# Performance work log

Measured on AMD Instinct MI355X. Metric: run time of the kernel, lower is better.

The kernel has to match this reference:

```python
import jax, jax.numpy as jnp
import numpy as np

N = 50000
E_G = 600000
E_K = 500000
IN_FEATS = 64
H = 128
C = 2
# calculate_theta2(d=2): Bernstein polynomial coefficients (ascending powers)
THETAS_G = [[3.0, -3.0, 0.75], [0.0, 3.0, -1.5], [0.0, 0.0, 0.75]]
THETAS_K = [[1.0, 1.0, 1.0]] * 3


def _xavier(key, shape):
    fan_in, fan_out = shape[1], shape[0]
    lim = float(np.sqrt(6.0 / (fan_in + fan_out)))
    return jax.random.uniform(key, shape, jnp.float32, -lim, lim)


def setup_inputs() -> dict:
    key = jax.random.key(0)
    ks = jax.random.split(key, 32)
    inp = {
        "x": jax.random.normal(ks[0], (N, IN_FEATS), jnp.float32),
        "src_g": jax.random.randint(ks[1], (E_G,), 0, N, jnp.int32),
        "dst_g": jax.random.randint(ks[2], (E_G,), 0, N, jnp.int32),
        "src_k": jax.random.randint(ks[3], (E_K,), 0, N, jnp.int32),
        "dst_k": jax.random.randint(ks[4], (E_K,), 0, N, jnp.int32),
        # input MLP
        "W1": _xavier(ks[5], (H, IN_FEATS)), "b1": jnp.zeros((H,), jnp.float32),
        "W2": _xavier(ks[6], (H, H)), "b2": jnp.zeros((H,), jnp.float32),
        # 3 PolyConvs on main graph: learnable_diag [3,3,H], linear [3,H,H]+bias
        "diag_g": jax.random.uniform(ks[7], (3, 3, H), jnp.float32),
        "Wc_g": jnp.stack([_xavier(ks[8 + i], (H, H)) for i in range(3)]),
        "bc_g": jnp.zeros((3, H), jnp.float32),
        # 3 PolyConvs on knn graph
        "diag_k": jax.random.uniform(ks[11], (3, 3, H), jnp.float32),
        "Wc_k": jnp.stack([_xavier(ks[12 + i], (H, H)) for i in range(3)]),
        "bc_k": jnp.zeros((3, H), jnp.float32),
        # fusion linears (3H -> H)
        "W3": _xavier(ks[15], (H, 3 * H)), "b3": jnp.zeros((H,), jnp.float32),
        "Wk": _xavier(ks[16], (H, 3 * H)), "bk": jnp.zeros((H,), jnp.float32),
        # ComponentAttention: Linear(H,H)+Tanh+Linear(H,1,no bias)
        "Wa1": _xavier(ks[17], (H, H)), "ba1": jnp.zeros((H,), jnp.float32),
        "Wa2": _xavier(ks[18], (1, H)),
        # classifier
        "W4": _xavier(ks[19], (C, H)), "b4": jnp.zeros((C,), jnp.float32),
    }
    return inp


def _dinvsqrt(dst, n):
    deg = jax.ops.segment_sum(jnp.ones(dst.shape, jnp.float32), dst, num_segments=n)
    return jnp.clip(deg, 1.0, None) ** -0.5  # [N]


def _poly_conv(feat, src, dst, dinv, theta, diag, W, b, n):
    # h = linear(theta[0]*feat * diag[0]); then k-1 Laplacian hops
    h = jnp.dot((theta[0] * feat) * diag[0], W.T) + b
    for k in range(1, len(theta)):
        m = feat * dinv  # [N,H]
        agg = jax.ops.segment_sum(m[src], dst, num_segments=n)  # SpMM
        feat = feat - (agg * dinv) * diag[k]
        h = h + theta[k] * feat
    return h


def reference(x, src_g, dst_g, src_k, dst_k, W1, b1, W2, b2, diag_g, Wc_g, bc_g,
              diag_k, Wc_k, bc_k, W3, b3, Wk, bk, Wa1, ba1, Wa2, W4, b4):
    dinv_g = _dinvsqrt(dst_g, N)[:, None]
    dinv_k = _dinvsqrt(dst_k, N)[:, None]

    h = jax.nn.relu(jnp.dot(x, W1.T) + b1)
    h = jax.nn.relu(jnp.dot(h, W2.T) + b2)

    h_o = jnp.concatenate(
        [_poly_conv(h, src_g, dst_g, dinv_g, THETAS_G[i], diag_g[i], Wc_g[i], bc_g[i], N)
         for i in range(3)], axis=-1)
    h_o = jax.nn.relu(jnp.dot(h_o, W3.T) + b3)

    h_knn = jnp.concatenate(
        [_poly_conv(h, src_k, dst_k, dinv_k, THETAS_K[i], diag_k[i], Wc_k[i], bc_k[i], N)
         for i in range(3)], axis=-1)
    h_knn = jax.nn.relu(jnp.dot(h_knn, Wk.T) + bk)

    z = jnp.stack([h_o, h_knn], axis=1)  # [N,2,H]
    w = jnp.dot(jnp.tanh(jnp.dot(z, Wa1.T) + ba1), Wa2.T)  # [N,2,1]
    beta = jax.nn.softmax(w.mean(axis=0), axis=0)  # [2,1]
    emb = (beta[None] * z).sum(axis=1)  # [N,H]

    logits = jnp.dot(emb, W4.T) + b4
    return (logits, emb)
```

## Files before the change

kernel.cpp:

```cpp
#include <hip/hip_runtime.h>
#include <math.h>

#define NN 50000
#define EG 600000
#define EK 500000
#define H 128
#define INF 64
#define NB 196

#define GRID 512

struct Theta9 { float t[9]; };

__device__ __forceinline__ float f4_at(const float4& v, int i) {
  return i == 0 ? v.x : i == 1 ? v.y : i == 2 ? v.z : v.w;
}
__device__ __forceinline__ void fma4(float4& a, float s, const float4& w) {
  a.x += s * w.x; a.y += s * w.y; a.z += s * w.z; a.w += s * w.w;
}
__device__ __forceinline__ float4 relu4(float4 a) {
  a.x = fmaxf(a.x, 0.f); a.y = fmaxf(a.y, 0.f);
  a.z = fmaxf(a.z, 0.f); a.w = fmaxf(a.w, 0.f);
  return a;
}
__device__ __forceinline__ float fast_tanh(float x) {
  float a = fabsf(x);
  float t = __expf(-2.f * a);
  float r = (1.f - t) * __builtin_amdgcn_rcpf(1.f + t);
  return copysignf(r, x);
}
__device__ __forceinline__ float dot_tanh4(const float4& w2, const float4& a) {
  return w2.x * fast_tanh(a.x) + w2.y * fast_tanh(a.y) +
         w2.z * fast_tanh(a.z) + w2.w * fast_tanh(a.w);
}

__global__ __launch_bounds__(256) void k_hist(const int* __restrict__ dg,
    const int* __restrict__ dk, int* __restrict__ cg, int* __restrict__ ck) {
  __shared__ int h[512];
  int t = threadIdx.x;
  h[t] = 0; h[t + 256] = 0;
  __syncthreads();
  for (int e = blockIdx.x * 256 + t; e < EG; e += gridDim.x * 256) {
    atomicAdd(&h[dg[e] >> 8], 1);
    if (e < EK) atomicAdd(&h[256 + (dk[e] >> 8)], 1);
  }
  __syncthreads();
  if (t < NB) {
    if (h[t]) atomicAdd(&cg[t], h[t]);
    if (h[256 + t]) atomicAdd(&ck[t], h[256 + t]);
  }
}

__global__ __launch_bounds__(256) void k_bscan(const int* __restrict__ cg,
    const int* __restrict__ ck, int* __restrict__ bg, int* __restrict__ bk,
    int* __restrict__ curg, int* __restrict__ curk,
    int* __restrict__ rpg, int* __restrict__ rpk) {
  __shared__ int sg[256], sk[256];
  int t = threadIdx.x;
  int vg = (t < NB) ? cg[t] : 0;
  int vk = (t < NB) ? ck[t] : 0;
  sg[t] = vg; sk[t] = vk;
  __syncthreads();
  for (int d = 1; d < 256; d <<= 1) {
    int ug = (t >= d) ? sg[t - d] : 0;
    int uk = (t >= d) ? sk[t - d] : 0;
    __syncthreads();
    sg[t] += ug; sk[t] += uk;
    __syncthreads();
  }
  int eg = sg[t] - vg, ek = sk[t] - vk;
  if (t < NB) {
    bg[t] = eg; bk[t] = ek;
    curg[t] = eg; curk[t] = ek;
  }
  if (t == NB - 1) {
    bg[NB] = eg + vg; bk[NB] = ek + vk;
    rpg[NN] = eg + vg; rpk[NN] = ek + vk;
  }
}

template<int E>
__global__ __launch_bounds__(256) void k_part(const int* __restrict__ src,
    const int* __restrict__ dst, int* __restrict__ gcur, int2* __restrict__ ebuf) {
  __shared__ int hist[NB], lbase[NB], cur[NB];
  int t = threadIdx.x;
  int CH = (E + gridDim.x - 1) / gridDim.x;
  int b0 = blockIdx.x * CH;
  int b1 = min(E, b0 + CH);
  if (t < NB) hist[t] = 0;
  __syncthreads();
  for (int e = b0 + t; e < b1; e += 256) atomicAdd(&hist[dst[e] >> 8], 1);
  __syncthreads();
  if (t < NB && hist[t]) lbase[t] = atomicAdd(&gcur[t], hist[t]);
  __syncthreads();
  if (t < NB) cur[t] = 0;
  __syncthreads();
  for (int e = b0 + t; e < b1; e += 256) {
    int d = dst[e];
    int b = d >> 8;
    int r = atomicAdd(&cur[b], 1);
    ebuf[lbase[b] + r] = make_int2(src[e], d);
  }
}

__global__ __launch_bounds__(256) void k_bcsr(const int2* __restrict__ ebuf,
    const int* __restrict__ bbase, int* __restrict__ rp, int* __restrict__ adj,
    float* __restrict__ dinv) {
  __shared__ int hist[256], incl[256], cur[256];
  int t = threadIdx.x, b = blockIdx.x;
  int beg = bbase[b], end = bbase[b + 1];
  int node0 = b << 8;
  int nvalid = min(256, NN - node0);
  hist[t] = 0;
  __syncthreads();
  for (int i = beg + t; i < end; i += 256) atomicAdd(&hist[ebuf[i].y - node0], 1);
  __syncthreads();
  incl[t] = hist[t];
  __syncthreads();
  for (int d = 1; d < 256; d <<= 1) {
    int u = (t >= d) ? incl[t - d] : 0;
    __syncthreads();
    incl[t] += u;
    __syncthreads();
  }
  int excl = incl[t] - hist[t];
  if (t < nvalid) {
    rp[node0 + t] = beg + excl;
    int dg = hist[t]; if (dg < 1) dg = 1;
    dinv[node0 + t] = rsqrtf((float)dg);
  }
  cur[t] = 0;
  incl[t] = excl;
  __syncthreads();
  for (int i = beg + t; i < end; i += 256) {
    int2 ed = ebuf[i];
    int d = ed.y - node0;
    int r = atomicAdd(&cur[d], 1);
    adj[beg + incl[d] + r] = ed.x;
  }
}

__global__ __launch_bounds__(256) void k_transpose(const float* __restrict__ A,
    float* __restrict__ At, int R, int C) {
  int i = blockIdx.x * 256 + threadIdx.x;
  if (i < R * C) {
    int r = i / C, c = i % C;
    At[c * R + r] = A[i];
  }
}

__global__ __launch_bounds__(256) void k_genmat(const float* __restrict__ diag,
    const float* __restrict__ Wc, const float* __restrict__ W3, Theta9 th,
    float* __restrict__ A, float* __restrict__ B, float* __restrict__ C) {
  int id = blockIdx.x * 256 + threadIdx.x;
  int k = id >> 7, j = id & 127;
  float a = 0.f, b = 0.f, c = 0.f;
  for (int i = 0; i < 3; i++) {
    float t0 = th.t[i * 3 + 0], t1 = th.t[i * 3 + 1], t2 = th.t[i * 3 + 2];
    float d0 = diag[(i * 3 + 0) * H + k];
    float d1 = diag[(i * 3 + 1) * H + k];
    float d2 = diag[(i * 3 + 2) * H + k];
    float ci = t0 * d0;
    float alpha = t1 + t2;
    float beta  = -((t1 + t2) * d1 + t2 * d2);
    float gamma = t2 * d1 * d2;
    float w3kj = W3[j * 384 + i * H + k];
    if (ci != 0.f) {
      const float* Wi = Wc + i * H * H;
      float g = 0.f;
      for (int m = 0; m < H; m++)
        g += Wi[m * H + k] * W3[j * 384 + i * H + m];
      a += ci * g;
    }
    a += alpha * w3kj;
    b += beta * w3kj;
    c += gamma * w3kj;
  }
  A[id] = a; B[id] = b; C[id] = c;
}

__global__ __launch_bounds__(256) void k_genbias(const float* __restrict__ bc,
    const float* __restrict__ W3, const float* __restrict__ b3, float* __restrict__ bias) {
  int j = threadIdx.x;
  float s = b3[j];
  for (int i = 0; i < 3; i++)
    for (int m = 0; m < H; m++)
      s += bc[i * H + m] * W3[j * 384 + i * H + m];
  bias[j] = s;
}

__device__ __forceinline__ void accum_tile(const float* __restrict__ X, int t,
    const float* __restrict__ wlds, int lane, float4* a) {
  int n0 = t * 6;
  const float* x0 = X + (size_t)n0 * H;
  if (n0 + 6 <= NN) {
    float4 xa[6], xb[6];
#pragma unroll
    for (int i = 0; i < 6; i++) xa[i] = *(const float4*)(x0 + (size_t)i * H);
    for (int k = 0; k < H; k += 4) {
      int kn = (k + 4 < H) ? (k + 4) : k;
#pragma unroll
      for (int i = 0; i < 6; i++)
        xb[i] = *(const float4*)(x0 + (size_t)i * H + kn);
#pragma unroll
      for (int kk = 0; kk < 4; kk++) {
        float4 w = *(const float4*)(wlds + (k + kk) * H + lane * 4);
#pragma unroll
        for (int i = 0; i < 6; i++) fma4(a[i], f4_at(xa[i], kk), w);
      }
#pragma unroll
      for (int i = 0; i < 6; i++) xa[i] = xb[i];
    }
  } else {
    int nv = NN - n0;
    for (int k = 0; k < H; k += 4) {
      float4 xv[6];
#pragma unroll
      for (int i = 0; i < 6; i++)
        xv[i] = (i < nv) ? *(const float4*)(x0 + (size_t)i * H + k)
                         : make_float4(0.f, 0.f, 0.f, 0.f);
#pragma unroll
      for (int kk = 0; kk < 4; kk++) {
        float4 w = *(const float4*)(wlds + (k + kk) * H + lane * 4);
#pragma unroll
        for (int i = 0; i < 6; i++) fma4(a[i], f4_at(xv[i], kk), w);
      }
    }
  }
}

__device__ __forceinline__ void write_tile(float* __restrict__ Y, int t, int lane,
    float4* a) {
  int n0 = t * 6;
  int nv = min(6, NN - n0);
  float* y = Y + (size_t)n0 * H + lane * 4;
#pragma unroll
  for (int i = 0; i < 6; i++) {
    if (i < nv) *(float4*)(y + (size_t)i * H) = relu4(a[i]);
  }
}

__global__ __launch_bounds__(512) void k_gemm64(const float* __restrict__ X,
    const float* __restrict__ Wt, const float* __restrict__ bias,
    float* __restrict__ Y) {
  __shared__ float wlds[INF * H];
#pragma unroll
  for (int i = 0; i < 4; i++) {
    int idx = (threadIdx.x + i * 512) * 4;
    *(float4*)(wlds + idx) = *(const float4*)(Wt + idx);
  }
  __syncthreads();
  const int lane = threadIdx.x & 31;
  const int g = (threadIdx.x >> 5) * gridDim.x + blockIdx.x;
  const int n0 = g * 4;
  if (n0 >= NN) return;
  const int nv = min(4, NN - n0);
  float4 bb = *(const float4*)(bias + lane * 4);
  float4 a[4];
#pragma unroll
  for (int i = 0; i < 4; i++) a[i] = bb;
  const float* x0 = X + (size_t)n0 * INF;
  if (nv == 4) {
    for (int k = 0; k < INF; k += 4) {
      float4 xv[4];
#pragma unroll
      for (int i = 0; i < 4; i++)
        xv[i] = *(const float4*)(x0 + (size_t)i * INF + k);
#pragma unroll
      for (int kk = 0; kk < 4; kk++) {
        float4 w = *(const float4*)(wlds + (k + kk) * H + lane * 4);
#pragma unroll
        for (int i = 0; i < 4; i++) fma4(a[i], f4_at(xv[i], kk), w);
      }
    }
  } else {
    for (int k = 0; k < INF; k += 4) {
      float4 xv[4];
#pragma unroll
      for (int i = 0; i < 4; i++)
        xv[i] = (i < nv) ? *(const float4*)(x0 + (size_t)i * INF + k)
                         : make_float4(0.f, 0.f, 0.f, 0.f);
#pragma unroll
      for (int kk = 0; kk < 4; kk++) {
        float4 w = *(const float4*)(wlds + (k + kk) * H + lane * 4);
#pragma unroll
        for (int i = 0; i < 4; i++) fma4(a[i], f4_at(xv[i], kk), w);
      }
    }
  }
  float* y = Y + (size_t)n0 * H + lane * 4;
#pragma unroll
  for (int i = 0; i < 4; i++)
    if (i < nv) *(float4*)(y + (size_t)i * H) = relu4(a[i]);
}

__global__ __launch_bounds__(512) void k_gemmH(const float* __restrict__ X,
    const float* __restrict__ Wt, const float* __restrict__ bias,
    float* __restrict__ Y) {
  __shared__ float wlds[H * H];
#pragma unroll
  for (int i = 0; i < 8; i++) {
    int idx = (threadIdx.x + i * 512) * 4;
    *(float4*)(wlds + idx) = *(const float4*)(Wt + idx);
  }
  __syncthreads();
  const int lane = threadIdx.x & 31;
  float4 bb = *(const float4*)(bias + lane * 4);
  const int NT = (NN + 5) / 6;
  const int g0 = (threadIdx.x >> 5) * gridDim.x + blockIdx.x;
  const int stride = gridDim.x * 16;
  for (int t = g0; t < NT; t += stride) {
    float4 a[6];
#pragma unroll
    for (int i = 0; i < 6; i++) a[i] = bb;
    accum_tile(X, t, wlds, lane, a);
    write_tile(Y, t, lane, a);
  }
}

__global__ __launch_bounds__(512) void k_lin3f(const float* __restrict__ X0,
    const float* __restrict__ X1, const float* __restrict__ X2,
    const float* __restrict__ A, const float* __restrict__ B,
    const float* __restrict__ C, const float* __restrict__ bias,
    float* __restrict__ Y) {
  __shared__ float wlds[H * H];
  const int lane = threadIdx.x & 31;
  const int g0 = (threadIdx.x >> 5) * gridDim.x + blockIdx.x;
  const int NG = gridDim.x * 16;
  const int NT = (NN + 5) / 6;
  const int t0 = g0, t1 = g0 + NG;
  float4 bb = *(const float4*)(bias + lane * 4);
  float4 a0[6], a1[6];
#pragma unroll
  for (int i = 0; i < 6; i++) { a0[i] = bb; a1[i] = bb; }

#define PHASE(W, X)                                                      \
  {                                                                      \
    __syncthreads();                                                     \
    _Pragma("unroll")                                                    \
    for (int i = 0; i < 8; i++) {                                        \
      int idx = (threadIdx.x + i * 512) * 4;                             \
      *(float4*)(wlds + idx) = *(const float4*)((W) + idx);              \
    }                                                                    \
    __syncthreads();                                                     \
    accum_tile((X), t0, wlds, lane, a0);                                 \
    if (t1 < NT) accum_tile((X), t1, wlds, lane, a1);                    \
  }

  PHASE(A, X0)
  PHASE(B, X1)
  PHASE(C, X2)
#undef PHASE

  write_tile(Y, t0, lane, a0);
  if (t1 < NT) write_tile(Y, t1, lane, a1);
}

__global__ __launch_bounds__(512) void k_attn(const float* __restrict__ Ho,
    const float* __restrict__ Hk, const float* __restrict__ Wa1t,
    const float* __restrict__ ba1, const float* __restrict__ Wa2,
    float* __restrict__ sums) {
  __shared__ float wlds[H * H];
#pragma unroll
  for (int i = 0; i < 8; i++) {
    int idx = (threadIdx.x + i * 512) * 4;
    *(float4*)(wlds + idx) = *(const float4*)(Wa1t + idx);
  }
  __syncthreads();
  const int lane = threadIdx.x & 31;
  float4 bb = *(const float4*)(ba1 + lane * 4);
  float4 w2 = *(const float4*)(Wa2 + lane * 4);
  const int g0 = (threadIdx.x >> 5) * gridDim.x + blockIdx.x;
  const int stride = gridDim.x * 16;
  float po = 0.f, pk = 0.f;
  for (int t = g0; t < NN / 4; t += stride) {
    int n0 = t * 4;
    const float* ho = Ho + (size_t)n0 * H;
    const float* hk = Hk + (size_t)n0 * H;
    float4 ao[4], ak[4];
#pragma unroll
    for (int i = 0; i < 4; i++) { ao[i] = bb; ak[i] = bb; }
    for (int k = 0; k < H; k += 4) {
      float4 xo[4], xk[4];
#pragma unroll
      for (int i = 0; i < 4; i++) {
        xo[i] = *(const float4*)(ho + (size_t)i * H + k);
        xk[i] = *(const float4*)(hk + (size_t)i * H + k);
      }
#pragma unroll
      for (int kk = 0; kk < 4; kk++) {
        float4 w = *(const float4*)(wlds + (k + kk) * H + lane * 4);
#pragma unroll
        for (int i = 0; i < 4; i++) {
          fma4(ao[i], f4_at(xo[i], kk), w);
          fma4(ak[i], f4_at(xk[i], kk), w);
        }
      }
    }
#pragma unroll
    for (int i = 0; i < 4; i++) {
      po += dot_tanh4(w2, ao[i]);
      pk += dot_tanh4(w2, ak[i]);
    }
  }
  for (int d = 32; d > 0; d >>= 1) {
    po += __shfl_down(po, d, 64);
    pk += __shfl_down(pk, d, 64);
  }
  __syncthreads();
  int wv = threadIdx.x >> 6;
  if ((threadIdx.x & 63) == 0) { wlds[wv] = po; wlds[8 + wv] = pk; }
  __syncthreads();
  if (threadIdx.x == 0) {
    float so = 0.f, sk = 0.f;
    for (int i = 0; i < 8; i++) { so += wlds[i]; sk += wlds[8 + i]; }
    atomicAdd(&sums[0], so);
    atomicAdd(&sums[1], sk);
  }
}

__global__ __launch_bounds__(256) void k_spmm(const float* __restrict__ X,
    const float* __restrict__ dinv, const int* __restrict__ rp,
    const int* __restrict__ adj, float* __restrict__ Y) {
  int g = blockIdx.x * blockDim.x + threadIdx.x;
  int n = g >> 5, lane = g & 31;
  if (n >= NN) return;
  float4 acc = make_float4(0.f, 0.f, 0.f, 0.f);
  int beg = rp[n], end = rp[n + 1];
  const float* Xl = X + lane * 4;
  int e = beg;
  for (; e + 8 <= end; e += 8) {
    int s[8];
#pragma unroll
    for (int j = 0; j < 8; j++) s[j] = adj[e + j];
    float d[8];
#pragma unroll
    for (int j = 0; j < 8; j++) d[j] = dinv[s[j]];
    float4 v[8];
#pragma unroll
    for (int j = 0; j < 8; j++) v[j] = *(const float4*)(Xl + (size_t)s[j] * H);
#pragma unroll
    for (int j = 0; j < 8; j++) fma4(acc, d[j], v[j]);
  }
  for (; e + 4 <= end; e += 4) {
    int s0 = adj[e], s1 = adj[e + 1], s2 = adj[e + 2], s3 = adj[e + 3];
    float d0 = dinv[s0], d1 = dinv[s1], d2 = dinv[s2], d3 = dinv[s3];
    float4 v0 = *(const float4*)(Xl + (size_t)s0 * H);
    float4 v1 = *(const float4*)(Xl + (size_t)s1 * H);
    float4 v2 = *(const float4*)(Xl + (size_t)s2 * H);
    float4 v3 = *(const float4*)(Xl + (size_t)s3 * H);
    fma4(acc, d0, v0);
    fma4(acc, d1, v1);
    fma4(acc, d2, v2);
    fma4(acc, d3, v3);
  }
  for (; e < end; e++) {
    int s = adj[e];
    fma4(acc, dinv[s], *(const float4*)(Xl + (size_t)s * H));
  }
  float dn = dinv[n];
  acc.x *= dn; acc.y *= dn; acc.z *= dn; acc.w *= dn;
  *(float4*)(Y + (size_t)n * H + lane * 4) = acc;
}

__global__ __launch_bounds__(256) void k_final(const float* __restrict__ Ho,
    const float* __restrict__ Hk, const float* __restrict__ sums,
    const float* __restrict__ W4, const float* __restrict__ b4,
    float* __restrict__ out) {
  int g = blockIdx.x * blockDim.x + threadIdx.x;
  int n = g >> 5, lane = g & 31;
  if (n >= NN) return;
  float mo = sums[0] * (1.f / NN);
  float mk = sums[1] * (1.f / NN);
  float mx = fmaxf(mo, mk);
  float eo = __expf(mo - mx), ek = __expf(mk - mx);
  float inv = 1.f / (eo + ek);
  float bo = eo * inv, bk2 = ek * inv;
  float4 ho = *(const float4*)(Ho + (size_t)n * H + lane * 4);
  float4 hk = *(const float4*)(Hk + (size_t)n * H + lane * 4);
  float4 emb;
  emb.x = bo * ho.x + bk2 * hk.x;
  emb.y = bo * ho.y + bk2 * hk.y;
  emb.z = bo * ho.z + bk2 * hk.z;
  emb.w = bo * ho.w + bk2 * hk.w;
  *(float4*)(out + 2 * NN + (size_t)n * H + lane * 4) = emb;
  float4 w0 = *(const float4*)(W4 + lane * 4);
  float4 w1 = *(const float4*)(W4 + H + lane * 4);
  float p0 = emb.x * w0.x + emb.y * w0.y + emb.z * w0.z + emb.w * w0.w;
  float p1 = emb.x * w1.x + emb.y * w1.y + emb.z * w1.z + emb.w * w1.w;
  for (int d = 16; d > 0; d >>= 1) {
    p0 += __shfl_down(p0, d, 32);
    p1 += __shfl_down(p1, d, 32);
  }
  if (lane == 0) {
    out[n * 2 + 0] = p0 + b4[0];
    out[n * 2 + 1] = p1 + b4[1];
  }
}

extern "C" void kernel_launch(void* const* d_in, const int* in_sizes, int n_in,
                              void* d_out, int out_size, void* d_ws, size_t ws_size,
                              hipStream_t stream) {
  const float* x      = (const float*)d_in[0];
  const int*   src_g  = (const int*)d_in[1];
  const int*   dst_g  = (const int*)d_in[2];
  const int*   src_k  = (const int*)d_in[3];
  const int*   dst_k  = (const int*)d_in[4];
  const float* W1     = (const float*)d_in[5];
  const float* b1     = (const float*)d_in[6];
  const float* W2     = (const float*)d_in[7];
  const float* b2     = (const float*)d_in[8];
  const float* diag_g = (const float*)d_in[9];
  const float* Wc_g   = (const float*)d_in[10];
  const float* bc_g   = (const float*)d_in[11];
  const float* diag_k = (const float*)d_in[12];
  const float* Wc_k   = (const float*)d_in[13];
  const float* bc_k   = (const float*)d_in[14];
  const float* W3     = (const float*)d_in[15];
  const float* b3     = (const float*)d_in[16];
  const float* Wk     = (const float*)d_in[17];
  const float* bk     = (const float*)d_in[18];
  const float* Wa1    = (const float*)d_in[19];
  const float* ba1    = (const float*)d_in[20];
  const float* Wa2    = (const float*)d_in[21];
  const float* W4     = (const float*)d_in[22];
  const float* b4     = (const float*)d_in[23];
  float* out = (float*)d_out;

  char* base = (char*)d_ws;
  size_t off = 0;
  auto alloc = [&](size_t bytes) -> char* {
    char* r = base + off;
    off = (off + bytes + 255) & ~(size_t)255;
    return r;
  };
  int* bcnt_g = (int*)alloc(256 * 4);
  int* bcnt_k = (int*)alloc(256 * 4);
  float* sums = (float*)alloc(256);
  size_t zero_bytes = off;

  int* bbase_g = (int*)alloc((NB + 1) * 4);
  int* bbase_k = (int*)alloc((NB + 1) * 4);
  int* bcur_g  = (int*)alloc(NB * 4);
  int* bcur_k  = (int*)alloc(NB * 4);
  int* rp_g    = (int*)alloc((NN + 1) * 4);
  int* rp_k    = (int*)alloc((NN + 1) * 4);
  int2* ebuf_g = (int2*)alloc((size_t)EG * 8);
  int2* ebuf_k = (int2*)alloc((size_t)EK * 8);
  int* adj_g   = (int*)alloc(EG * 4);
  int* adj_k   = (int*)alloc(EK * 4);
  float* dinv_g = (float*)alloc(NN * 4);
  float* dinv_k = (float*)alloc(NN * 4);
  float* Wt1  = (float*)alloc(INF * H * 4);
  float* Wt2  = (float*)alloc(H * H * 4);
  float* Wa1t = (float*)alloc(H * H * 4);
  float* Ag = (float*)alloc(H * H * 4);
  float* Bg = (float*)alloc(H * H * 4);
  float* Cg = (float*)alloc(H * H * 4);
  float* biasg = (float*)alloc(H * 4);
  float* Ak = (float*)alloc(H * H * 4);
  float* Bk = (float*)alloc(H * H * 4);
  float* Ck = (float*)alloc(H * H * 4);
  float* biask = (float*)alloc(H * 4);
  float* B0 = (float*)alloc((size_t)NN * H * 4);
  float* B1 = (float*)alloc((size_t)NN * H * 4);
  float* B2 = (float*)alloc((size_t)NN * H * 4);
  float* B3 = (float*)alloc((size_t)NN * H * 4);
  float* B4 = (float*)alloc((size_t)NN * H * 4);
  (void)ws_size; (void)in_sizes; (void)n_in; (void)out_size;

  hipMemsetAsync(d_ws, 0, zero_bytes, stream);

  const int GB = NN * 32 / 256;

  k_hist<<<512, 256, 0, stream>>>(dst_g, dst_k, bcnt_g, bcnt_k);
  k_bscan<<<1, 256, 0, stream>>>(bcnt_g, bcnt_k, bbase_g, bbase_k,
                                 bcur_g, bcur_k, rp_g, rp_k);
  k_part<EG><<<512, 256, 0, stream>>>(src_g, dst_g, bcur_g, ebuf_g);
  k_part<EK><<<512, 256, 0, stream>>>(src_k, dst_k, bcur_k, ebuf_k);
  k_bcsr<<<NB, 256, 0, stream>>>(ebuf_g, bbase_g, rp_g, adj_g, dinv_g);
  k_bcsr<<<NB, 256, 0, stream>>>(ebuf_k, bbase_k, rp_k, adj_k, dinv_k);

  k_transpose<<<(H * INF + 255) / 256, 256, 0, stream>>>(W1, Wt1, H, INF);
  k_transpose<<<(H * H + 255) / 256, 256, 0, stream>>>(W2, Wt2, H, H);
  k_transpose<<<(H * H + 255) / 256, 256, 0, stream>>>(Wa1, Wa1t, H, H);
  Theta9 thG = {{3.f, -3.f, 0.75f, 0.f, 3.f, -1.5f, 0.f, 0.f, 0.75f}};
  Theta9 thK = {{1.f, 1.f, 1.f, 1.f, 1.f, 1.f, 1.f, 1.f, 1.f}};
  k_genmat<<<64, 256, 0, stream>>>(diag_g, Wc_g, W3, thG, Ag, Bg, Cg);
  k_genmat<<<64, 256, 0, stream>>>(diag_k, Wc_k, Wk, thK, Ak, Bk, Ck);
  k_genbias<<<1, 128, 0, stream>>>(bc_g, W3, b3, biasg);
  k_genbias<<<1, 128, 0, stream>>>(bc_k, Wk, bk, biask);

  k_gemm64<<<1024, 512, 0, stream>>>(x, Wt1, b1, B0);
  k_gemmH<<<GRID, 512, 0, stream>>>(B0, Wt2, b2, B1);

  k_spmm<<<GB, 256, 0, stream>>>(B1, dinv_g, rp_g, adj_g, B2);
  k_spmm<<<GB, 256, 0, stream>>>(B2, dinv_g, rp_g, adj_g, B3);
  k_lin3f<<<GRID, 512, 0, stream>>>(B1, B2, B3, Ag, Bg, Cg, biasg, B0);

  k_spmm<<<GB, 256, 0, stream>>>(B1, dinv_k, rp_k, adj_k, B2);
  k_spmm<<<GB, 256, 0, stream>>>(B2, dinv_k, rp_k, adj_k, B3);
  k_lin3f<<<GRID, 512, 0, stream>>>(B1, B2, B3, Ak, Bk, Ck, biask, B4);

  k_attn<<<GRID, 512, 0, stream>>>(B0, B4, Wa1t, ba1, Wa2, sums);
  k_final<<<GB, 256, 0, stream>>>(B0, B4, sums, W4, b4, out);
}
```

Baseline: 684.8 us.

## Halve LDS weight staging and shrink row tiles to raise GEMM occupancy

```diff
diff --git a/kernel.cpp b/kernel.cpp
--- a/kernel.cpp
+++ b/kernel.cpp
@@ -9,6 +9,7 @@
 #define NB 196
 
 #define GRID 512
+#define GRID3 1024
 
 struct Theta9 { float t[9]; };
 
@@ -189,54 +190,57 @@
   bias[j] = s;
 }
 
-__device__ __forceinline__ void accum_tile(const float* __restrict__ X, int t,
-    const float* __restrict__ wlds, int lane, float4* a) {
-  int n0 = t * 6;
-  const float* x0 = X + (size_t)n0 * H;
-  if (n0 + 6 <= NN) {
-    float4 xa[6], xb[6];
-#pragma unroll
-    for (int i = 0; i < 6; i++) xa[i] = *(const float4*)(x0 + (size_t)i * H);
-    for (int k = 0; k < H; k += 4) {
-      int kn = (k + 4 < H) ? (k + 4) : k;
-#pragma unroll
-      for (int i = 0; i < 6; i++)
-        xb[i] = *(const float4*)(x0 + (size_t)i * H + kn);
+__device__ __forceinline__ void accum3(const float* __restrict__ X, int t,
+    const float* __restrict__ wlds, int lane, float4* a, int k0) {
+  int n0 = t * 3;
+  const float* x0 = X + (size_t)n0 * H + k0;
+  if (n0 + 3 <= NN) {
+    for (int k = 0; k < 64; k += 4) {
+      float4 xv[3];
+#pragma unroll
+      for (int i = 0; i < 3; i++)
+        xv[i] = *(const float4*)(x0 + (size_t)i * H + k);
 #pragma unroll
       for (int kk = 0; kk < 4; kk++) {
         float4 w = *(const float4*)(wlds + (k + kk) * H + lane * 4);
 #pragma unroll
-        for (int i = 0; i < 6; i++) fma4(a[i], f4_at(xa[i], kk), w);
+        for (int i = 0; i < 3; i++) fma4(a[i], f4_at(xv[i], kk), w);
       }
-#pragma unroll
-      for (int i = 0; i < 6; i++) xa[i] = xb[i];
     }
   } else {
     int nv = NN - n0;
-    for (int k = 0; k < H; k += 4) {
-      float4 xv[6];
-#pragma unroll
-      for (int i = 0; i < 6; i++)
+    for (int k = 0; k < 64; k += 4) {
+      float4 xv[3];
+#pragma unroll
+      for (int i = 0; i < 3; i++)
         xv[i] = (i < nv) ? *(const float4*)(x0 + (size_t)i * H + k)
                          : make_float4(0.f, 0.f, 0.f, 0.f);
 #pragma unroll
       for (int kk = 0; kk < 4; kk++) {
         float4 w = *(const float4*)(wlds + (k + kk) * H + lane * 4);
 #pragma unroll
-        for (int i = 0; i < 6; i++) fma4(a[i], f4_at(xv[i], kk), w);
+        for (int i = 0; i < 3; i++) fma4(a[i], f4_at(xv[i], kk), w);
       }
     }
   }
 }
 
-__device__ __forceinline__ void write_tile(float* __restrict__ Y, int t, int lane,
+__device__ __forceinline__ void write3(float* __restrict__ Y, int t, int lane,
     float4* a) {
-  int n0 = t * 6;
-  int nv = min(6, NN - n0);
+  int n0 = t * 3;
+  int nv = min(3, NN - n0);
   float* y = Y + (size_t)n0 * H + lane * 4;
 #pragma unroll
-  for (int i = 0; i < 6; i++) {
+  for (int i = 0; i < 3; i++)
     if (i < nv) *(float4*)(y + (size_t)i * H) = relu4(a[i]);
+}
+
+__device__ __forceinline__ void stage_half(float* __restrict__ wlds,
+    const float* __restrict__ W) {
+#pragma unroll
+  for (int i = 0; i < 4; i++) {
+    int idx = (threadIdx.x + i * 512) * 4;
+    *(float4*)(wlds + idx) = *(const float4*)(W + idx);
   }
 }
 
@@ -297,25 +301,25 @@
 __global__ __launch_bounds__(512) void k_gemmH(const float* __restrict__ X,
     const float* __restrict__ Wt, const float* __restrict__ bias,
     float* __restrict__ Y) {
-  __shared__ float wlds[H * H];
-#pragma unroll
-  for (int i = 0; i < 8; i++) {
-    int idx = (threadIdx.x + i * 512) * 4;
-    *(float4*)(wlds + idx) = *(const float4*)(Wt + idx);
-  }
-  __syncthreads();
+  __shared__ float wlds[64 * H];
   const int lane = threadIdx.x & 31;
+  const int g0 = (threadIdx.x >> 5) * gridDim.x + blockIdx.x;
+  const int NG = gridDim.x * 16;
+  const int NT = (NN + 2) / 3;
+  const int t0 = g0, t1 = g0 + NG;
   float4 bb = *(const float4*)(bias + lane * 4);
-  const int NT = (NN + 5) / 6;
-  const int g0 = (threadIdx.x >> 5) * gridDim.x + blockIdx.x;
-  const int stride = gridDim.x * 16;
-  for (int t = g0; t < NT; t += stride) {
-    float4 a[6];
-#pragma unroll
-    for (int i = 0; i < 6; i++) a[i] = bb;
-    accum_tile(X, t, wlds, lane, a);
-    write_tile(Y, t, lane, a);
-  }
+  float4 a0[3], a1[3];
+#pragma unroll
+  for (int i = 0; i < 3; i++) { a0[i] = bb; a1[i] = bb; }
+  for (int h = 0; h < 2; h++) {
+    __syncthreads();
+    stage_half(wlds, Wt + h * 64 * H);
+    __syncthreads();
+    accum3(X, t0, wlds, lane, a0, h * 64);
+    if (t1 < NT) accum3(X, t1, wlds, lane, a1, h * 64);
+  }
+  write3(Y, t0, lane, a0);
+  if (t1 < NT) write3(Y, t1, lane, a1);
 }
 
 __global__ __launch_bounds__(512) void k_lin3f(const float* __restrict__ X0,
@@ -323,28 +327,24 @@
     const float* __restrict__ A, const float* __restrict__ B,
     const float* __restrict__ C, const float* __restrict__ bias,
     float* __restrict__ Y) {
-  __shared__ float wlds[H * H];
+  __shared__ float wlds[64 * H];
   const int lane = threadIdx.x & 31;
   const int g0 = (threadIdx.x >> 5) * gridDim.x + blockIdx.x;
   const int NG = gridDim.x * 16;
-  const int NT = (NN + 5) / 6;
+  const int NT = (NN + 2) / 3;
   const int t0 = g0, t1 = g0 + NG;
   float4 bb = *(const float4*)(bias + lane * 4);
-  float4 a0[6], a1[6];
-#pragma unroll
-  for (int i = 0; i < 6; i++) { a0[i] = bb; a1[i] = bb; }
+  float4 a0[3], a1[3];
+#pragma unroll
+  for (int i = 0; i < 3; i++) { a0[i] = bb; a1[i] = bb; }
 
 #define PHASE(W, X)                                                      \
-  {                                                                      \
+  for (int h = 0; h < 2; h++) {                                          \
     __syncthreads();                                                     \
-    _Pragma("unroll")                                                    \
-    for (int i = 0; i < 8; i++) {                                        \
-      int idx = (threadIdx.x + i * 512) * 4;                             \
-      *(float4*)(wlds + idx) = *(const float4*)((W) + idx);              \
-    }                                                                    \
+    stage_half(wlds, (W) + h * 64 * H);                                  \
     __syncthreads();                                                     \
-    accum_tile((X), t0, wlds, lane, a0);                                 \
-    if (t1 < NT) accum_tile((X), t1, wlds, lane, a1);                    \
+    accum3((X), t0, wlds, lane, a0, h * 64);                             \
+    if (t1 < NT) accum3((X), t1, wlds, lane, a1, h * 64);                \
   }
 
   PHASE(A, X0)
@@ -352,8 +352,8 @@
   PHASE(C, X2)
 #undef PHASE
 
-  write_tile(Y, t0, lane, a0);
-  if (t1 < NT) write_tile(Y, t1, lane, a1);
+  write3(Y, t0, lane, a0);
+  if (t1 < NT) write3(Y, t1, lane, a1);
 }
 
 __global__ __launch_bounds__(512) void k_attn(const float* __restrict__ Ho,
@@ -592,15 +592,15 @@
   k_genbias<<<1, 128, 0, stream>>>(bc_k, Wk, bk, biask);
 
   k_gemm64<<<1024, 512, 0, stream>>>(x, Wt1, b1, B0);
-  k_gemmH<<<GRID, 512, 0, stream>>>(B0, Wt2, b2, B1);
+  k_gemmH<<<GRID3, 512, 0, stream>>>(B0, Wt2, b2, B1);
 
   k_spmm<<<GB, 256, 0, stream>>>(B1, dinv_g, rp_g, adj_g, B2);
   k_spmm<<<GB, 256, 0, stream>>>(B2, dinv_g, rp_g, adj_g, B3);
-  k_lin3f<<<GRID, 512, 0, stream>>>(B1, B2, B3, Ag, Bg, Cg, biasg, B0);
+  k_lin3f<<<GRID3, 512, 0, stream>>>(B1, B2, B3, Ag, Bg, Cg, biasg, B0);
 
   k_spmm<<<GB, 256, 0, stream>>>(B1, dinv_k, rp_k, adj_k, B2);
   k_spmm<<<GB, 256, 0, stream>>>(B2, dinv_k, rp_k, adj_k, B3);
-  k_lin3f<<<GRID, 512, 0, stream>>>(B1, B2, B3, Ak, Bk, Ck, biask, B4);
+  k_lin3f<<<GRID3, 512, 0, stream>>>(B1, B2, B3, Ak, Bk, Ck, biask, B4);
 
   k_attn<<<GRID, 512, 0, stream>>>(B0, B4, Wa1t, ba1, Wa2, sums);
   k_final<<<GB, 256, 0, stream>>>(B0, B4, sums, W4, b4, out);
```

Measured after the change: 878.8 us. 28.3% more time.
